# Performance work log

Measured on AMD Instinct MI355X. Metric: run time of the kernel, lower is better.

Reference implementation:

```python
import jax, jax.numpy as jnp
import numpy as np

N_NODES = 100000
N_EDGES = 1600000
F_IN, HIDDEN, N_CLASS = 64, 48, 40


def setup_inputs() -> dict:
    key = jax.random.key(0)
    ks = jax.random.split(key, 9)
    def glorot(k, fi, fo):
        s = (6.0 / (fi + fo)) ** 0.5
        return jax.random.uniform(k, (fi, fo), jnp.float32, -s, s)
    return {
        "x": jax.random.normal(ks[0], (N_NODES, F_IN), jnp.float32),
        "edge_index": jax.random.randint(ks[1], (2, N_EDGES), 0, N_NODES, jnp.int64),
        "edge_weight": jax.random.uniform(ks[2], (N_EDGES,), jnp.float32),
        "W1": glorot(ks[3], F_IN, HIDDEN),   # ARMAConv init_weight (K=1)
        "V1": glorot(ks[4], F_IN, HIDDEN),   # ARMAConv root_weight
        "b1": jnp.zeros((HIDDEN,), jnp.float32),
        "W2": glorot(ks[5], HIDDEN, N_CLASS),
        "V2": glorot(ks[6], HIDDEN, N_CLASS),
        "b2": jnp.zeros((N_CLASS,), jnp.float32),
    }


def _arma_conv(x, W, V, b, src, dst, norm, num_nodes):
    # out = ReLU( A_norm @ (x @ W) + x @ V + b )   (num_stacks=1, num_layers=1)
    h = x @ W                                   # [N, F_out]
    msg = h[src] * norm[:, None]                # gather + scale  [E, F_out]
    agg = jax.ops.segment_sum(msg, dst, num_segments=num_nodes)  # scatter-add
    return jax.nn.relu(agg + x @ V + b)


def reference(x, edge_index, edge_weight, W1, V1, b1, W2, V2, b2):
    num_nodes = x.shape[0]
    src, dst = edge_index[0], edge_index[1]
    # gcn_norm, add_self_loops=False: D^{-1/2} A D^{-1/2}
    deg = jax.ops.segment_sum(edge_weight, dst, num_segments=num_nodes)
    dinv = jnp.where(deg > 0, jax.lax.rsqrt(jnp.where(deg > 0, deg, 1.0)), 0.0)
    norm = dinv[src] * edge_weight * dinv[dst]
    # eval mode: input dropout is identity
    h = _arma_conv(x, W1, V1, b1, src, dst, norm, num_nodes)
    h = _arma_conv(h, W2, V2, b2, src, dst, norm, num_nodes)
    return jax.nn.log_softmax(h, axis=-1)
```

## Files before the change

### kernel.cpp

```cpp
#include <hip/hip_runtime.h>
#include <math.h>


constexpr int F_IN = 64;
constexpr int HIDDEN = 48;
constexpr int N_CLASS = 40;
constexpr int CHUNK = 8192;
constexpr int BIN_SHIFT = 9;
constexpr int CSR_CAP = 12288;

typedef __attribute__((ext_vector_type(8))) short bf16x8;
typedef __attribute__((ext_vector_type(4))) float f32x4;

__device__ __forceinline__ short bfr(float f) {
    unsigned u = __float_as_uint(f);
    return (short)((u + 0x7fffu + ((u >> 16) & 1u)) >> 16);
}
__device__ __forceinline__ unsigned pack_bf2(float a, float b) {
    unsigned ua = __float_as_uint(a), ub = __float_as_uint(b);
    ua = (ua + 0x7fffu + ((ua >> 16) & 1u)) >> 16;
    ub = (ub + 0x7fffu + ((ub >> 16) & 1u)) >> 16;
    return ua | (ub << 16);
}
__device__ __forceinline__ float2 unpack_bf2(unsigned u) {
    return make_float2(__uint_as_float(u << 16), __uint_as_float(u & 0xffff0000u));
}
__device__ __forceinline__ bf16x8 cvt8(float4 f0, float4 f1) {
    bf16x8 r;
    r[0] = bfr(f0.x); r[1] = bfr(f0.y); r[2] = bfr(f0.z); r[3] = bfr(f0.w);
    r[4] = bfr(f1.x); r[5] = bfr(f1.y); r[6] = bfr(f1.z); r[7] = bfr(f1.w);
    return r;
}

__device__ __forceinline__ void mfma_gemm1_body(char* smem, const float* __restrict__ X,
                                                const float* __restrict__ W,
                                                const float* __restrict__ V,
                                                const float* __restrict__ b,
                                                unsigned* __restrict__ XWp,
                                                float* __restrict__ AGG, int N, int gb,
                                                int tid) {
    short* sWT = (short*)smem;
    float* ep = (float*)(smem + 12288);
    for (int i = tid; i < 96 * 64; i += 256) {
        int c = i >> 6, k = i & 63;
        float v = (c < 48) ? W[k * 48 + c] : V[k * 48 + (c - 48)];
        sWT[i] = bfr(v);
    }
    __syncthreads();

    int lane = tid & 63, wv = tid >> 6;
    int m = lane & 15, quad = lane >> 4;
    int nb0 = gb * 64;
    int n = nb0 + wv * 16 + m;

    bf16x8 a0, a1;
    if (n < N) {
        const float4* xr = (const float4*)(X + (size_t)n * 64 + quad * 8);
        a0 = cvt8(xr[0], xr[1]);
        const float4* xr2 = (const float4*)(X + (size_t)n * 64 + 32 + quad * 8);
        a1 = cvt8(xr2[0], xr2[1]);
    } else {
        for (int j = 0; j < 8; ++j) { a0[j] = 0; a1[j] = 0; }
    }

    f32x4 acc[6];
#pragma unroll
    for (int ct = 0; ct < 6; ++ct) acc[ct] = (f32x4){0.f, 0.f, 0.f, 0.f};
#pragma unroll
    for (int ct = 0; ct < 6; ++ct) {
        bf16x8 b0 = *(const bf16x8*)(sWT + (ct * 16 + m) * 64 + quad * 8);
        bf16x8 b1 = *(const bf16x8*)(sWT + (ct * 16 + m) * 64 + 32 + quad * 8);
        acc[ct] = __builtin_amdgcn_mfma_f32_16x16x32_bf16(a0, b0, acc[ct], 0, 0, 0);
        acc[ct] = __builtin_amdgcn_mfma_f32_16x16x32_bf16(a1, b1, acc[ct], 0, 0, 0);
    }
#pragma unroll
    for (int ct = 0; ct < 6; ++ct)
#pragma unroll
        for (int r = 0; r < 4; ++r)
            ep[(wv * 16 + quad * 4 + r) * 96 + ct * 16 + m] = acc[ct][r];
    __syncthreads();
    for (int i = tid; i < 64 * 24; i += 256) {
        int r = i / 24, c2 = i - r * 24;
        int node = nb0 + r;
        if (node >= N) continue;
        float w0 = ep[r * 96 + 2 * c2], w1 = ep[r * 96 + 2 * c2 + 1];
        XWp[node * 24 + c2] = pack_bf2(w0, w1);
        float v0 = ep[r * 96 + 48 + 2 * c2], v1 = ep[r * 96 + 48 + 2 * c2 + 1];
        float2 bb = ((const float2*)b)[c2];
        ((float2*)AGG)[node * 24 + c2] = make_float2(v0 + bb.x, v1 + bb.y);
    }
}

__global__ __launch_bounds__(256) void count_gemm1(
    const int* __restrict__ dst, int* __restrict__ binCnt, int E, int nCountBlocks,
    const float* __restrict__ X, const float* __restrict__ W,
    const float* __restrict__ V, const float* __restrict__ b,
    unsigned* __restrict__ XWp, float* __restrict__ AGG, int N) {
    __shared__ char smem[36864];
    if ((int)blockIdx.x < nCountBlocks) {
        int* hist = (int*)smem;
        int tid = threadIdx.x;
        hist[tid] = 0;
        __syncthreads();
        long long e0 = (long long)blockIdx.x * CHUNK;
        int M = (int)min((long long)CHUNK, (long long)E - e0);
        for (int i = tid; i < M; i += 256) atomicAdd(&hist[dst[e0 + i] >> BIN_SHIFT], 1);
        __syncthreads();
        atomicAdd(&binCnt[tid], hist[tid]);
    } else {
        mfma_gemm1_body(smem, X, W, V, b, XWp, AGG, N,
                        (int)blockIdx.x - nCountBlocks, (int)threadIdx.x);
    }
}

__global__ void scan_bins(const int* __restrict__ binCnt, int* __restrict__ binStart,
                          int* __restrict__ binCursor, int* __restrict__ rowPtr,
                          int E, int N) {
    __shared__ int s[256];
    int t = threadIdx.x;
    int v = binCnt[t];
    s[t] = v;
    __syncthreads();
#pragma unroll
    for (int o = 1; o < 256; o <<= 1) {
        int u = (t >= o) ? s[t - o] : 0;
        __syncthreads();
        s[t] += u;
        __syncthreads();
    }
    int excl = s[t] - v;
    binStart[t] = excl;
    binCursor[t] = excl;
    if (t == 0) {
        binStart[256] = E;
        rowPtr[N] = E;
    }
}

__global__ void binscatter(const int* __restrict__ src, const int* __restrict__ dst,
                           const float* __restrict__ w, int* __restrict__ binCursor,
                           int2* __restrict__ binned, int E) {
    __shared__ int sx[CHUNK];
    __shared__ int sw[CHUNK];
    __shared__ unsigned char sbin[CHUNK];
    __shared__ int hist[256];
    int tid = threadIdx.x;
    hist[tid] = 0;
    __syncthreads();
    long long e0 = (long long)blockIdx.x * CHUNK;
    int M = (int)min((long long)CHUNK, (long long)E - e0);
    for (int i = tid; i < M; i += 256) {
        int d = dst[e0 + i];
        int bn = d >> BIN_SHIFT;
        sx[i] = ((d & 511) << 17) | src[e0 + i];
        sw[i] = __float_as_int(w[e0 + i]);
        sbin[i] = (unsigned char)bn;
        atomicAdd(&hist[bn], 1);
    }
    __syncthreads();
    int base = atomicAdd(&binCursor[tid], hist[tid]);
    __syncthreads();
    hist[tid] = base;
    __syncthreads();
    for (int i = tid; i < M; i += 256) {
        int p = atomicAdd(&hist[sbin[i]], 1);
        binned[p] = make_int2(sx[i], sw[i]);
    }
}

__global__ __launch_bounds__(512) void build_csr(const int2* __restrict__ binned,
                                                 const int* __restrict__ binStart,
                                                 int* __restrict__ rowPtr,
                                                 float* __restrict__ dinv,
                                                 int2* __restrict__ csr, int N) {
    __shared__ int sx[CSR_CAP];
    __shared__ int sw[CSR_CAP];
    __shared__ int cntL[512];
    __shared__ float degL[512];
    __shared__ int scanL[512];
    int b = blockIdx.x, tid = threadIdx.x;
    int e0 = binStart[b], e1 = binStart[b + 1], M = e1 - e0;
    cntL[tid] = 0;
    degL[tid] = 0.f;
    __syncthreads();
    bool fits = (M <= CSR_CAP);
    for (int i = tid; i < M; i += 512) {
        int2 p = binned[e0 + i];
        if (fits) { sx[i] = p.x; sw[i] = p.y; }
        int dl = ((unsigned)p.x) >> 17;
        atomicAdd(&cntL[dl], 1);
        atomicAdd(&degL[dl], __int_as_float(p.y));
    }
    __syncthreads();
    int v = cntL[tid];
    scanL[tid] = v;
    __syncthreads();
#pragma unroll
    for (int o = 1; o < 512; o <<= 1) {
        int u = (tid >= o) ? scanL[tid - o] : 0;
        __syncthreads();
        scanL[tid] += u;
        __syncthreads();
    }
    int excl = scanL[tid] - v;
    int node = (b << BIN_SHIFT) + tid;
    float dg = degL[tid];
    float dv = dg > 0.f ? rsqrtf(dg) : 0.f;
    if (node < N) {
        rowPtr[node] = e0 + excl;
        dinv[node] = dv;
    }
    cntL[tid] = e0 + excl;
    degL[tid] = dv;
    __syncthreads();
    for (int i = tid; i < M; i += 512) {
        int px, pw;
        if (fits) { px = sx[i]; pw = sw[i]; }
        else { int2 p = binned[e0 + i]; px = p.x; pw = p.y; }
        int dl = ((unsigned)px) >> 17;
        int pos = atomicAdd(&cntL[dl], 1);
        float wn = __int_as_float(pw) * degL[dl];
        csr[pos] = make_int2(px & 0x1FFFF, __float_as_int(wn));
    }
}

template <int C2>
__global__ void scale_xw(unsigned* __restrict__ XWp, const float* __restrict__ dinv,
                         int total) {
    int t = blockIdx.x * blockDim.x + threadIdx.x;
    if (t >= total) return;
    float dv = dinv[t / C2];
    float2 u = unpack_bf2(XWp[t]);
    XWp[t] = pack_bf2(u.x * dv, u.y * dv);
}

__global__ __launch_bounds__(256) void gemm2_kernel(
    const float* __restrict__ X, const float* __restrict__ W,
    const float* __restrict__ V, const float* __restrict__ b,
    const float* __restrict__ dinv, unsigned* __restrict__ XWp,
    float* __restrict__ AGG, int N) {
    __shared__ char smem[30720];
    short* sWT = (short*)smem;
    float* ep = (float*)(smem + 10240);
    int tid = threadIdx.x;
    for (int i = tid; i < 80 * 64; i += 256) {
        int c = i >> 6, k = i & 63;
        float v = 0.f;
        if (k < 48) v = (c < 40) ? W[k * 40 + c] : V[k * 40 + (c - 40)];
        sWT[i] = bfr(v);
    }
    __syncthreads();

    int lane = tid & 63, wv = tid >> 6;
    int m = lane & 15, quad = lane >> 4;
    int nb0 = (int)blockIdx.x * 64;
    int n = nb0 + wv * 16 + m;

    bf16x8 a0, a1;
    if (n < N) {
        const float4* xr = (const float4*)(X + (size_t)n * 48 + quad * 8);
        float4 f0 = xr[0], f1 = xr[1];
        f0.x = fmaxf(f0.x, 0.f); f0.y = fmaxf(f0.y, 0.f);
        f0.z = fmaxf(f0.z, 0.f); f0.w = fmaxf(f0.w, 0.f);
        f1.x = fmaxf(f1.x, 0.f); f1.y = fmaxf(f1.y, 0.f);
        f1.z = fmaxf(f1.z, 0.f); f1.w = fmaxf(f1.w, 0.f);
        a0 = cvt8(f0, f1);
        if (quad < 2) {
            const float4* xr2 = (const float4*)(X + (size_t)n * 48 + 32 + quad * 8);
            float4 g0 = xr2[0], g1 = xr2[1];
            g0.x = fmaxf(g0.x, 0.f); g0.y = fmaxf(g0.y, 0.f);
            g0.z = fmaxf(g0.z, 0.f); g0.w = fmaxf(g0.w, 0.f);
            g1.x = fmaxf(g1.x, 0.f); g1.y = fmaxf(g1.y, 0.f);
            g1.z = fmaxf(g1.z, 0.f); g1.w = fmaxf(g1.w, 0.f);
            a1 = cvt8(g0, g1);
        } else {
            for (int j = 0; j < 8; ++j) a1[j] = 0;
        }
    } else {
        for (int j = 0; j < 8; ++j) { a0[j] = 0; a1[j] = 0; }
    }

    f32x4 acc[5];
#pragma unroll
    for (int ct = 0; ct < 5; ++ct) acc[ct] = (f32x4){0.f, 0.f, 0.f, 0.f};
#pragma unroll
    for (int ct = 0; ct < 5; ++ct) {
        bf16x8 b0 = *(const bf16x8*)(sWT + (ct * 16 + m) * 64 + quad * 8);
        bf16x8 b1 = *(const bf16x8*)(sWT + (ct * 16 + m) * 64 + 32 + quad * 8);
        acc[ct] = __builtin_amdgcn_mfma_f32_16x16x32_bf16(a0, b0, acc[ct], 0, 0, 0);
        acc[ct] = __builtin_amdgcn_mfma_f32_16x16x32_bf16(a1, b1, acc[ct], 0, 0, 0);
    }
#pragma unroll
    for (int ct = 0; ct < 5; ++ct)
#pragma unroll
        for (int r = 0; r < 4; ++r)
            ep[(wv * 16 + quad * 4 + r) * 80 + ct * 16 + m] = acc[ct][r];
    __syncthreads();
    for (int i = tid; i < 64 * 20; i += 256) {
        int r = i / 20, c2 = i - r * 20;
        int node = nb0 + r;
        if (node >= N) continue;
        float dv = dinv[node];
        float w0 = ep[r * 80 + 2 * c2], w1 = ep[r * 80 + 2 * c2 + 1];
        XWp[node * 20 + c2] = pack_bf2(w0 * dv, w1 * dv);
        float v0 = ep[r * 80 + 40 + 2 * c2], v1 = ep[r * 80 + 40 + 2 * c2 + 1];
        float2 bb = ((const float2*)b)[c2];
        ((float2*)AGG)[node * 20 + c2] = make_float2(v0 + bb.x, v1 + bb.y);
    }
}

template <int C2>
__device__ __forceinline__ float2 row_accum(const unsigned* __restrict__ XWp,
                                            const int2* __restrict__ csr, int j,
                                            int end, int c2, float2 s) {
    for (; j + 4 <= end; j += 4) {
        int2 p0 = csr[j], p1 = csr[j + 1], p2 = csr[j + 2], p3 = csr[j + 3];
        unsigned u0 = XWp[p0.x * C2 + c2];
        unsigned u1 = XWp[p1.x * C2 + c2];
        unsigned u2 = XWp[p2.x * C2 + c2];
        unsigned u3 = XWp[p3.x * C2 + c2];
        float2 x0 = unpack_bf2(u0), x1 = unpack_bf2(u1);
        float2 x2 = unpack_bf2(u2), x3 = unpack_bf2(u3);
        float n0 = __int_as_float(p0.y), n1 = __int_as_float(p1.y);
        float n2 = __int_as_float(p2.y), n3 = __int_as_float(p3.y);
        s.x = fmaf(x0.x, n0, s.x); s.y = fmaf(x0.y, n0, s.y);
        s.x = fmaf(x1.x, n1, s.x); s.y = fmaf(x1.y, n1, s.y);
        s.x = fmaf(x2.x, n2, s.x); s.y = fmaf(x2.y, n2, s.y);
        s.x = fmaf(x3.x, n3, s.x); s.y = fmaf(x3.y, n3, s.y);
    }
    for (; j < end; ++j) {
        int2 p = csr[j];
        float2 xw = unpack_bf2(XWp[p.x * C2 + c2]);
        float nr = __int_as_float(p.y);
        s.x = fmaf(xw.x, nr, s.x);
        s.y = fmaf(xw.y, nr, s.y);
    }
    return s;
}

template <int C>
__global__ void pull_agg(const unsigned* __restrict__ XWp, const int2* __restrict__ csr,
                         const int* __restrict__ rowPtr, float* __restrict__ AGG, int N) {
    constexpr int C2 = C / 2;
    int t = blockIdx.x * blockDim.x + threadIdx.x;
    if (t >= N * C2) return;
    int n = t / C2, c2 = t - n * C2;
    float2 s = ((const float2*)AGG)[t];
    s = row_accum<C2>(XWp, csr, rowPtr[n], rowPtr[n + 1], c2, s);
    ((float2*)AGG)[t] = s;
}

__global__ __launch_bounds__(320) void pull_ls(const unsigned* __restrict__ XWp,
                                               const int2* __restrict__ csr,
                                               const int* __restrict__ rowPtr,
                                               const float* __restrict__ AGGin,
                                               float* __restrict__ out, int N) {
    constexpr int C2 = N_CLASS / 2;
    __shared__ float2 sbuf[16 * C2];
    __shared__ float sl[16];
    int tid = threadIdx.x;
    int nl = tid / C2, c2 = tid - nl * C2;
    int n = blockIdx.x * 16 + nl;
    float2 s = make_float2(0.f, 0.f);
    if (n < N) {
        s = ((const float2*)AGGin)[n * C2 + c2];
        s = row_accum<C2>(XWp, csr, rowPtr[n], rowPtr[n + 1], c2, s);
    }
    sbuf[tid] = s;
    __syncthreads();
    if (tid < 16) {
        const float2* row = sbuf + tid * C2;
        float m = 0.f;
        for (int k = 0; k < C2; ++k) {
            float2 v = row[k];
            m = fmaxf(m, fmaxf(v.x, v.y));
        }
        float sum = 0.f;
        for (int k = 0; k < C2; ++k) {
            float2 v = row[k];
            sum += expf(fmaxf(v.x, 0.f) - m) + expf(fmaxf(v.y, 0.f) - m);
        }
        sl[tid] = m + logf(sum);
    }
    __syncthreads();
    if (n < N) {
        float l = sl[nl];
        ((float2*)out)[n * C2 + c2] =
            make_float2(fmaxf(s.x, 0.f) - l, fmaxf(s.y, 0.f) - l);
    }
}

extern "C" void kernel_launch(void* const* d_in, const int* in_sizes, int n_in,
                              void* d_out, int out_size, void* d_ws, size_t ws_size,
                              hipStream_t stream) {
    const float* x  = (const float*)d_in[0];
    const int*   ei = (const int*)d_in[1];
    const float* ew = (const float*)d_in[2];
    const float* W1 = (const float*)d_in[3];
    const float* V1 = (const float*)d_in[4];
    const float* b1 = (const float*)d_in[5];
    const float* W2 = (const float*)d_in[6];
    const float* V2 = (const float*)d_in[7];
    const float* b2 = (const float*)d_in[8];
    float* out = (float*)d_out;

    const int N = in_sizes[0] / F_IN;
    const int E = in_sizes[2];
    const int* src = ei;
    const int* dst = ei + E;

    char* ws = (char*)d_ws;
    size_t off = 0;
    auto carve = [&](size_t bytes) {
        void* p = ws + off;
        off = (off + bytes + 255) & ~size_t(255);
        return p;
    };
    int*      binCnt    = (int*)carve(256 * 4);
    int*      binStart  = (int*)carve(257 * 4);
    int*      binCursor = (int*)carve(256 * 4);
    int*      rowPtr    = (int*)carve((size_t)(N + 1) * 4);
    float*    dinv      = (float*)carve((size_t)N * 4);
    int2*     binned    = (int2*)carve((size_t)E * 8);
    int2*     csr       = (int2*)carve((size_t)E * 8);
    unsigned* xW1p      = (unsigned*)carve((size_t)N * (HIDDEN / 2) * 4);
    float*    agg1      = (float*)carve((size_t)N * HIDDEN * 4);
    float*    agg2      = (float*)carve((size_t)N * N_CLASS * 4);
    unsigned* xW2p      = xW1p;

    const int B = 256;
    auto cdiv = [](long long a, long long b) { return (int)((a + b - 1) / b); };
    const int nChunks = cdiv(E, CHUNK);
    const int nBins = (N + (1 << BIN_SHIFT) - 1) >> BIN_SHIFT;
    const int nGemmBlocks = cdiv(N, 64);

    hipMemsetAsync(binCnt, 0, 256 * 4, stream);

    count_gemm1<<<nChunks + nGemmBlocks, B, 0, stream>>>(dst, binCnt, E, nChunks,
                                                         x, W1, V1, b1, xW1p, agg1, N);
    scan_bins<<<1, 256, 0, stream>>>(binCnt, binStart, binCursor, rowPtr, E, N);
    binscatter<<<nChunks, B, 0, stream>>>(src, dst, ew, binCursor, binned, E);
    build_csr<<<nBins, 512, 0, stream>>>(binned, binStart, rowPtr, dinv, csr, N);

    scale_xw<HIDDEN / 2><<<cdiv((long long)N * (HIDDEN / 2), B), B, 0, stream>>>(
        xW1p, dinv, N * (HIDDEN / 2));

    pull_agg<HIDDEN><<<cdiv((long long)N * (HIDDEN / 2), B), B, 0, stream>>>(
        xW1p, csr, rowPtr, agg1, N);

    gemm2_kernel<<<nGemmBlocks, B, 0, stream>>>(agg1, W2, V2, b2, dinv, xW2p, agg2, N);

    pull_ls<<<cdiv(N, 16), 320, 0, stream>>>(xW2p, csr, rowPtr, agg2, out, N);
}
```

Baseline: 294.4 us.

## Split gathered feature tables into column slabs and sweep slabs in persistent pull kernels

```diff
diff --git a/kernel.cpp b/kernel.cpp
--- a/kernel.cpp
+++ b/kernel.cpp
@@ -8,6 +8,8 @@
 constexpr int CHUNK = 8192;
 constexpr int BIN_SHIFT = 9;
 constexpr int CSR_CAP = 12288;
+constexpr int PULL_GRID = 1568;
+constexpr int P2TILES = 2;
 
 typedef __attribute__((ext_vector_type(8))) short bf16x8;
 typedef __attribute__((ext_vector_type(4))) float f32x4;
@@ -84,7 +86,8 @@
         int node = nb0 + r;
         if (node >= N) continue;
         float w0 = ep[r * 96 + 2 * c2], w1 = ep[r * 96 + 2 * c2 + 1];
-        XWp[node * 24 + c2] = pack_bf2(w0, w1);
+        int s = c2 >> 3, cc = c2 & 7;
+        XWp[((size_t)s * N + node) * 8 + cc] = pack_bf2(w0, w1);
         float v0 = ep[r * 96 + 48 + 2 * c2], v1 = ep[r * 96 + 48 + 2 * c2 + 1];
         float2 bb = ((const float2*)b)[c2];
         ((float2*)AGG)[node * 24 + c2] = make_float2(v0 + bb.x, v1 + bb.y);
@@ -224,12 +227,14 @@
     }
 }
 
-template <int C2>
 __global__ void scale_xw(unsigned* __restrict__ XWp, const float* __restrict__ dinv,
-                         int total) {
+                         int N) {
     int t = blockIdx.x * blockDim.x + threadIdx.x;
-    if (t >= total) return;
-    float dv = dinv[t / C2];
+    if (t >= N * 24) return;
+    int slabN8 = N * 8;
+    int s = t / slabN8;
+    int n = (t - s * slabN8) >> 3;
+    float dv = dinv[n];
     float2 u = unpack_bf2(XWp[t]);
     XWp[t] = pack_bf2(u.x * dv, u.y * dv);
 }
@@ -302,23 +307,26 @@
         if (node >= N) continue;
         float dv = dinv[node];
         float w0 = ep[r * 80 + 2 * c2], w1 = ep[r * 80 + 2 * c2 + 1];
-        XWp[node * 20 + c2] = pack_bf2(w0 * dv, w1 * dv);
+        unsigned pk = pack_bf2(w0 * dv, w1 * dv);
+        if (c2 < 8)       XWp[node * 8 + c2] = pk;
+        else if (c2 < 16) XWp[(size_t)N * 8 + node * 8 + (c2 - 8)] = pk;
+        else              XWp[(size_t)N * 16 + node * 4 + (c2 - 16)] = pk;
         float v0 = ep[r * 80 + 40 + 2 * c2], v1 = ep[r * 80 + 40 + 2 * c2 + 1];
         float2 bb = ((const float2*)b)[c2];
         ((float2*)AGG)[node * 20 + c2] = make_float2(v0 + bb.x, v1 + bb.y);
     }
 }
 
-template <int C2>
-__device__ __forceinline__ float2 row_accum(const unsigned* __restrict__ XWp,
-                                            const int2* __restrict__ csr, int j,
-                                            int end, int c2, float2 s) {
+template <int W>
+__device__ __forceinline__ float2 row_accumW(const unsigned* __restrict__ slab,
+                                             const int2* __restrict__ csr, int j,
+                                             int end, int c, float2 s) {
     for (; j + 4 <= end; j += 4) {
         int2 p0 = csr[j], p1 = csr[j + 1], p2 = csr[j + 2], p3 = csr[j + 3];
-        unsigned u0 = XWp[p0.x * C2 + c2];
-        unsigned u1 = XWp[p1.x * C2 + c2];
-        unsigned u2 = XWp[p2.x * C2 + c2];
-        unsigned u3 = XWp[p3.x * C2 + c2];
+        unsigned u0 = slab[p0.x * W + c];
+        unsigned u1 = slab[p1.x * W + c];
+        unsigned u2 = slab[p2.x * W + c];
+        unsigned u3 = slab[p3.x * W + c];
         float2 x0 = unpack_bf2(u0), x1 = unpack_bf2(u1);
         float2 x2 = unpack_bf2(u2), x3 = unpack_bf2(u3);
         float n0 = __int_as_float(p0.y), n1 = __int_as_float(p1.y);
@@ -330,7 +338,7 @@
     }
     for (; j < end; ++j) {
         int2 p = csr[j];
-        float2 xw = unpack_bf2(XWp[p.x * C2 + c2]);
+        float2 xw = unpack_bf2(slab[p.x * W + c]);
         float nr = __int_as_float(p.y);
         s.x = fmaf(xw.x, nr, s.x);
         s.y = fmaf(xw.y, nr, s.y);
@@ -338,55 +346,104 @@
     return s;
 }
 
-template <int C>
-__global__ void pull_agg(const unsigned* __restrict__ XWp, const int2* __restrict__ csr,
-                         const int* __restrict__ rowPtr, float* __restrict__ AGG, int N) {
-    constexpr int C2 = C / 2;
-    int t = blockIdx.x * blockDim.x + threadIdx.x;
-    if (t >= N * C2) return;
-    int n = t / C2, c2 = t - n * C2;
-    float2 s = ((const float2*)AGG)[t];
-    s = row_accum<C2>(XWp, csr, rowPtr[n], rowPtr[n + 1], c2, s);
-    ((float2*)AGG)[t] = s;
-}
-
-__global__ __launch_bounds__(320) void pull_ls(const unsigned* __restrict__ XWp,
-                                               const int2* __restrict__ csr,
-                                               const int* __restrict__ rowPtr,
-                                               const float* __restrict__ AGGin,
-                                               float* __restrict__ out, int N) {
-    constexpr int C2 = N_CLASS / 2;
-    __shared__ float2 sbuf[16 * C2];
-    __shared__ float sl[16];
+__global__ __launch_bounds__(256) void pull1(const unsigned* __restrict__ XWp,
+                                             const int2* __restrict__ csr,
+                                             const int* __restrict__ rowPtr,
+                                             float* __restrict__ AGG, int N,
+                                             int nTiles) {
     int tid = threadIdx.x;
-    int nl = tid / C2, c2 = tid - nl * C2;
-    int n = blockIdx.x * 16 + nl;
-    float2 s = make_float2(0.f, 0.f);
-    if (n < N) {
-        s = ((const float2*)AGGin)[n * C2 + c2];
-        s = row_accum<C2>(XWp, csr, rowPtr[n], rowPtr[n + 1], c2, s);
-    }
-    sbuf[tid] = s;
-    __syncthreads();
-    if (tid < 16) {
-        const float2* row = sbuf + tid * C2;
-        float m = 0.f;
-        for (int k = 0; k < C2; ++k) {
-            float2 v = row[k];
-            m = fmaxf(m, fmaxf(v.x, v.y));
+    int nl = tid >> 3, c = tid & 7;
+#pragma unroll
+    for (int s = 0; s < 3; ++s) {
+        const unsigned* slab = XWp + (size_t)s * N * 8;
+        int cp = s * 8 + c;
+        for (int tile = blockIdx.x; tile < nTiles; tile += gridDim.x) {
+            int n = tile * 32 + nl;
+            if (n >= N) continue;
+            int beg = rowPtr[n], end = rowPtr[n + 1];
+            float2 acc = ((const float2*)AGG)[n * 24 + cp];
+            acc = row_accumW<8>(slab, csr, beg, end, c, acc);
+            ((float2*)AGG)[n * 24 + cp] = acc;
         }
-        float sum = 0.f;
-        for (int k = 0; k < C2; ++k) {
-            float2 v = row[k];
-            sum += expf(fmaxf(v.x, 0.f) - m) + expf(fmaxf(v.y, 0.f) - m);
+    }
+}
+
+__global__ __launch_bounds__(256) void pull2_ls(const unsigned* __restrict__ XWp,
+                                                const int2* __restrict__ csr,
+                                                const int* __restrict__ rowPtr,
+                                                const float* __restrict__ AGGin,
+                                                float* __restrict__ out, int N,
+                                                int nTiles) {
+    __shared__ float2 sacc[P2TILES * 32 * 20];
+    __shared__ float sl[P2TILES * 32];
+    int tid = threadIdx.x;
+#pragma unroll
+    for (int tl = 0; tl < P2TILES; ++tl) {
+        int tile = blockIdx.x + tl * gridDim.x;
+        if (tile >= nTiles) break;
+        for (int i = tid; i < 32 * 20; i += 256) {
+            int nl = i / 20, c2 = i - nl * 20;
+            int n = tile * 32 + nl;
+            sacc[tl * 640 + i] =
+                (n < N) ? ((const float2*)AGGin)[n * 20 + c2] : make_float2(0.f, 0.f);
         }
-        sl[tid] = m + logf(sum);
-    }
-    __syncthreads();
-    if (n < N) {
-        float l = sl[nl];
-        ((float2*)out)[n * C2 + c2] =
-            make_float2(fmaxf(s.x, 0.f) - l, fmaxf(s.y, 0.f) - l);
+    }
+    __syncthreads();
+#pragma unroll
+    for (int s = 0; s < 3; ++s) {
+        int w = (s == 2) ? 4 : 8;
+        const unsigned* slab = XWp + (size_t)((s == 2) ? N * 16 : s * N * 8);
+        int nl = tid / w, c = tid - nl * w;
+        if (nl < 32) {
+#pragma unroll
+            for (int tl = 0; tl < P2TILES; ++tl) {
+                int tile = blockIdx.x + tl * gridDim.x;
+                if (tile >= nTiles) break;
+                int n = tile * 32 + nl;
+                if (n >= N) continue;
+                int beg = rowPtr[n], end = rowPtr[n + 1];
+                float2 acc = make_float2(0.f, 0.f);
+                acc = (w == 8) ? row_accumW<8>(slab, csr, beg, end, c, acc)
+                               : row_accumW<4>(slab, csr, beg, end, c, acc);
+                int cp = (s == 2) ? 16 + c : s * 8 + c;
+                float2* p = &sacc[tl * 640 + nl * 20 + cp];
+                *p = make_float2(p->x + acc.x, p->y + acc.y);
+            }
+        }
+    }
+    __syncthreads();
+    if (tid < P2TILES * 32) {
+        int tl = tid >> 5, nl = tid & 31;
+        int tile = blockIdx.x + tl * gridDim.x;
+        if (tile < nTiles) {
+            const float2* row = &sacc[tl * 640 + nl * 20];
+            float m = 0.f;
+            for (int k = 0; k < 20; ++k) {
+                float2 v = row[k];
+                m = fmaxf(m, fmaxf(v.x, v.y));
+            }
+            float sum = 0.f;
+            for (int k = 0; k < 20; ++k) {
+                float2 v = row[k];
+                sum += expf(fmaxf(v.x, 0.f) - m) + expf(fmaxf(v.y, 0.f) - m);
+            }
+            sl[tid] = m + logf(sum);
+        }
+    }
+    __syncthreads();
+#pragma unroll
+    for (int tl = 0; tl < P2TILES; ++tl) {
+        int tile = blockIdx.x + tl * gridDim.x;
+        if (tile >= nTiles) break;
+        for (int i = tid; i < 32 * 20; i += 256) {
+            int nl = i / 20, c2 = i - nl * 20;
+            int n = tile * 32 + nl;
+            if (n >= N) continue;
+            float l = sl[tl * 32 + nl];
+            float2 v = sacc[tl * 640 + i];
+            ((float2*)out)[n * 20 + c2] =
+                make_float2(fmaxf(v.x, 0.f) - l, fmaxf(v.y, 0.f) - l);
+        }
     }
 }
 
@@ -433,6 +490,7 @@
     const int nChunks = cdiv(E, CHUNK);
     const int nBins = (N + (1 << BIN_SHIFT) - 1) >> BIN_SHIFT;
     const int nGemmBlocks = cdiv(N, 64);
+    const int nTiles = cdiv(N, 32);
 
     hipMemsetAsync(binCnt, 0, 256 * 4, stream);
 
@@ -442,13 +500,11 @@
     binscatter<<<nChunks, B, 0, stream>>>(src, dst, ew, binCursor, binned, E);
     build_csr<<<nBins, 512, 0, stream>>>(binned, binStart, rowPtr, dinv, csr, N);
 
-    scale_xw<HIDDEN / 2><<<cdiv((long long)N * (HIDDEN / 2), B), B, 0, stream>>>(
-        xW1p, dinv, N * (HIDDEN / 2));
-
-    pull_agg<HIDDEN><<<cdiv((long long)N * (HIDDEN / 2), B), B, 0, stream>>>(
-        xW1p, csr, rowPtr, agg1, N);
+    scale_xw<<<cdiv((long long)N * 24, B), B, 0, stream>>>(xW1p, dinv, N);
+
+    pull1<<<PULL_GRID, B, 0, stream>>>(xW1p, csr, rowPtr, agg1, N, nTiles);
 
     gemm2_kernel<<<nGemmBlocks, B, 0, stream>>>(agg1, W2, V2, b2, dinv, xW2p, agg2, N);
 
-    pull_ls<<<cdiv(N, 16), 320, 0, stream>>>(xW2p, csr, rowPtr, agg2, out, N);
-}
+    pull2_ls<<<PULL_GRID, B, 0, stream>>>(xW2p, csr, rowPtr, agg2, out, N, nTiles);
+}
```

New measurement: 309.9 us. +5.2%, slower.

## Compress CSR entries to 32 bits and fuse layer-1 aggregation into GEMM2

Applied to the files above, without the earlier changes.

```diff
diff --git a/kernel.cpp b/kernel.cpp
--- a/kernel.cpp
+++ b/kernel.cpp
@@ -172,7 +172,7 @@
                                                  const int* __restrict__ binStart,
                                                  int* __restrict__ rowPtr,
                                                  float* __restrict__ dinv,
-                                                 int2* __restrict__ csr, int N) {
+                                                 unsigned* __restrict__ csr, int N) {
     __shared__ int sx[CSR_CAP];
     __shared__ int sw[CSR_CAP];
     __shared__ int cntL[512];
@@ -220,28 +220,61 @@
         int dl = ((unsigned)px) >> 17;
         int pos = atomicAdd(&cntL[dl], 1);
         float wn = __int_as_float(pw) * degL[dl];
-        csr[pos] = make_int2(px & 0x1FFFF, __float_as_int(wn));
-    }
-}
-
-template <int C2>
+        unsigned uw = __float_as_uint(wn);
+        uw = (uw + 0x7fffu + ((uw >> 16) & 1u)) >> 16;
+        csr[pos] = ((unsigned)(px & 0x1FFFF) << 15) | uw;
+    }
+}
+
 __global__ void scale_xw(unsigned* __restrict__ XWp, const float* __restrict__ dinv,
                          int total) {
     int t = blockIdx.x * blockDim.x + threadIdx.x;
     if (t >= total) return;
-    float dv = dinv[t / C2];
+    float dv = dinv[t / 24];
     float2 u = unpack_bf2(XWp[t]);
     XWp[t] = pack_bf2(u.x * dv, u.y * dv);
 }
 
-__global__ __launch_bounds__(256) void gemm2_kernel(
-    const float* __restrict__ X, const float* __restrict__ W,
-    const float* __restrict__ V, const float* __restrict__ b,
-    const float* __restrict__ dinv, unsigned* __restrict__ XWp,
-    float* __restrict__ AGG, int N) {
-    __shared__ char smem[30720];
-    short* sWT = (short*)smem;
-    float* ep = (float*)(smem + 10240);
+template <int W>
+__device__ __forceinline__ float2 row_accumC(const unsigned* __restrict__ XWp,
+                                             const unsigned* __restrict__ csr, int j,
+                                             int end, int c, float2 s) {
+    for (; j + 4 <= end; j += 4) {
+        unsigned p0 = csr[j], p1 = csr[j + 1], p2 = csr[j + 2], p3 = csr[j + 3];
+        unsigned u0 = XWp[(p0 >> 15) * W + c];
+        unsigned u1 = XWp[(p1 >> 15) * W + c];
+        unsigned u2 = XWp[(p2 >> 15) * W + c];
+        unsigned u3 = XWp[(p3 >> 15) * W + c];
+        float2 x0 = unpack_bf2(u0), x1 = unpack_bf2(u1);
+        float2 x2 = unpack_bf2(u2), x3 = unpack_bf2(u3);
+        float n0 = __uint_as_float((p0 & 0x7FFFu) << 16);
+        float n1 = __uint_as_float((p1 & 0x7FFFu) << 16);
+        float n2 = __uint_as_float((p2 & 0x7FFFu) << 16);
+        float n3 = __uint_as_float((p3 & 0x7FFFu) << 16);
+        s.x = fmaf(x0.x, n0, s.x); s.y = fmaf(x0.y, n0, s.y);
+        s.x = fmaf(x1.x, n1, s.x); s.y = fmaf(x1.y, n1, s.y);
+        s.x = fmaf(x2.x, n2, s.x); s.y = fmaf(x2.y, n2, s.y);
+        s.x = fmaf(x3.x, n3, s.x); s.y = fmaf(x3.y, n3, s.y);
+    }
+    for (; j < end; ++j) {
+        unsigned p = csr[j];
+        float2 xw = unpack_bf2(XWp[(p >> 15) * W + c]);
+        float nr = __uint_as_float((p & 0x7FFFu) << 16);
+        s.x = fmaf(xw.x, nr, s.x);
+        s.y = fmaf(xw.y, nr, s.y);
+    }
+    return s;
+}
+
+__global__ __launch_bounds__(256) void pull1_gemm2(
+    const unsigned* __restrict__ XW1p, const unsigned* __restrict__ csr,
+    const int* __restrict__ rowPtr, const float* __restrict__ AGG1in,
+    const float* __restrict__ W, const float* __restrict__ V,
+    const float* __restrict__ b, const float* __restrict__ dinv,
+    unsigned* __restrict__ XW2p, float* __restrict__ AGG2, int N) {
+    __shared__ short sWT[80 * 64];
+    __shared__ float sA[64 * 48];
+    __shared__ float ep[64 * 80];
     int tid = threadIdx.x;
     for (int i = tid; i < 80 * 64; i += 256) {
         int c = i >> 6, k = i & 63;
@@ -249,37 +282,35 @@
         if (k < 48) v = (c < 40) ? W[k * 40 + c] : V[k * 40 + (c - 40)];
         sWT[i] = bfr(v);
     }
-    __syncthreads();
-
+    int nb0 = (int)blockIdx.x * 64;
+    for (int i = tid; i < 64 * 24; i += 256) {
+        int nl = i / 24, c2 = i - nl * 24;
+        int n = nb0 + nl;
+        float2 acc = make_float2(0.f, 0.f);
+        if (n < N) {
+            acc = ((const float2*)AGG1in)[n * 24 + c2];
+            acc = row_accumC<24>(XW1p, csr, rowPtr[n], rowPtr[n + 1], c2, acc);
+        }
+        sA[nl * 48 + 2 * c2] = fmaxf(acc.x, 0.f);
+        sA[nl * 48 + 2 * c2 + 1] = fmaxf(acc.y, 0.f);
+    }
+    __syncthreads();
     int lane = tid & 63, wv = tid >> 6;
     int m = lane & 15, quad = lane >> 4;
-    int nb0 = (int)blockIdx.x * 64;
-    int n = nb0 + wv * 16 + m;
-
     bf16x8 a0, a1;
-    if (n < N) {
-        const float4* xr = (const float4*)(X + (size_t)n * 48 + quad * 8);
-        float4 f0 = xr[0], f1 = xr[1];
-        f0.x = fmaxf(f0.x, 0.f); f0.y = fmaxf(f0.y, 0.f);
-        f0.z = fmaxf(f0.z, 0.f); f0.w = fmaxf(f0.w, 0.f);
-        f1.x = fmaxf(f1.x, 0.f); f1.y = fmaxf(f1.y, 0.f);
-        f1.z = fmaxf(f1.z, 0.f); f1.w = fmaxf(f1.w, 0.f);
+    {
+        const float* ar = sA + (wv * 16 + m) * 48;
+        float4 f0 = *(const float4*)(ar + quad * 8);
+        float4 f1 = *(const float4*)(ar + quad * 8 + 4);
         a0 = cvt8(f0, f1);
         if (quad < 2) {
-            const float4* xr2 = (const float4*)(X + (size_t)n * 48 + 32 + quad * 8);
-            float4 g0 = xr2[0], g1 = xr2[1];
-            g0.x = fmaxf(g0.x, 0.f); g0.y = fmaxf(g0.y, 0.f);
-            g0.z = fmaxf(g0.z, 0.f); g0.w = fmaxf(g0.w, 0.f);
-            g1.x = fmaxf(g1.x, 0.f); g1.y = fmaxf(g1.y, 0.f);
-            g1.z = fmaxf(g1.z, 0.f); g1.w = fmaxf(g1.w, 0.f);
+            float4 g0 = *(const float4*)(ar + 32 + quad * 8);
+            float4 g1 = *(const float4*)(ar + 32 + quad * 8 + 4);
             a1 = cvt8(g0, g1);
         } else {
             for (int j = 0; j < 8; ++j) a1[j] = 0;
         }
-    } else {
-        for (int j = 0; j < 8; ++j) { a0[j] = 0; a1[j] = 0; }
-    }
-
+    }
     f32x4 acc[5];
 #pragma unroll
     for (int ct = 0; ct < 5; ++ct) acc[ct] = (f32x4){0.f, 0.f, 0.f, 0.f};
@@ -302,56 +333,15 @@
         if (node >= N) continue;
         float dv = dinv[node];
         float w0 = ep[r * 80 + 2 * c2], w1 = ep[r * 80 + 2 * c2 + 1];
-        XWp[node * 20 + c2] = pack_bf2(w0 * dv, w1 * dv);
+        XW2p[node * 20 + c2] = pack_bf2(w0 * dv, w1 * dv);
         float v0 = ep[r * 80 + 40 + 2 * c2], v1 = ep[r * 80 + 40 + 2 * c2 + 1];
         float2 bb = ((const float2*)b)[c2];
-        ((float2*)AGG)[node * 20 + c2] = make_float2(v0 + bb.x, v1 + bb.y);
-    }
-}
-
-template <int C2>
-__device__ __forceinline__ float2 row_accum(const unsigned* __restrict__ XWp,
-                                            const int2* __restrict__ csr, int j,
-                                            int end, int c2, float2 s) {
-    for (; j + 4 <= end; j += 4) {
-        int2 p0 = csr[j], p1 = csr[j + 1], p2 = csr[j + 2], p3 = csr[j + 3];
-        unsigned u0 = XWp[p0.x * C2 + c2];
-        unsigned u1 = XWp[p1.x * C2 + c2];
-        unsigned u2 = XWp[p2.x * C2 + c2];
-        unsigned u3 = XWp[p3.x * C2 + c2];
-        float2 x0 = unpack_bf2(u0), x1 = unpack_bf2(u1);
-        float2 x2 = unpack_bf2(u2), x3 = unpack_bf2(u3);
-        float n0 = __int_as_float(p0.y), n1 = __int_as_float(p1.y);
-        float n2 = __int_as_float(p2.y), n3 = __int_as_float(p3.y);
-        s.x = fmaf(x0.x, n0, s.x); s.y = fmaf(x0.y, n0, s.y);
-        s.x = fmaf(x1.x, n1, s.x); s.y = fmaf(x1.y, n1, s.y);
-        s.x = fmaf(x2.x, n2, s.x); s.y = fmaf(x2.y, n2, s.y);
-        s.x = fmaf(x3.x, n3, s.x); s.y = fmaf(x3.y, n3, s.y);
-    }
-    for (; j < end; ++j) {
-        int2 p = csr[j];
-        float2 xw = unpack_bf2(XWp[p.x * C2 + c2]);
-        float nr = __int_as_float(p.y);
-        s.x = fmaf(xw.x, nr, s.x);
-        s.y = fmaf(xw.y, nr, s.y);
-    }
-    return s;
-}
-
-template <int C>
-__global__ void pull_agg(const unsigned* __restrict__ XWp, const int2* __restrict__ csr,
-                         const int* __restrict__ rowPtr, float* __restrict__ AGG, int N) {
-    constexpr int C2 = C / 2;
-    int t = blockIdx.x * blockDim.x + threadIdx.x;
-    if (t >= N * C2) return;
-    int n = t / C2, c2 = t - n * C2;
-    float2 s = ((const float2*)AGG)[t];
-    s = row_accum<C2>(XWp, csr, rowPtr[n], rowPtr[n + 1], c2, s);
-    ((float2*)AGG)[t] = s;
+        ((float2*)AGG2)[node * 20 + c2] = make_float2(v0 + bb.x, v1 + bb.y);
+    }
 }
 
 __global__ __launch_bounds__(320) void pull_ls(const unsigned* __restrict__ XWp,
-                                               const int2* __restrict__ csr,
+                                               const unsigned* __restrict__ csr,
                                                const int* __restrict__ rowPtr,
                                                const float* __restrict__ AGGin,
                                                float* __restrict__ out, int N) {
@@ -364,7 +354,7 @@
     float2 s = make_float2(0.f, 0.f);
     if (n < N) {
         s = ((const float2*)AGGin)[n * C2 + c2];
-        s = row_accum<C2>(XWp, csr, rowPtr[n], rowPtr[n + 1], c2, s);
+        s = row_accumC<C2>(XWp, csr, rowPtr[n], rowPtr[n + 1], c2, s);
     }
     sbuf[tid] = s;
     __syncthreads();
@@ -422,11 +412,11 @@
     int*      rowPtr    = (int*)carve((size_t)(N + 1) * 4);
     float*    dinv      = (float*)carve((size_t)N * 4);
     int2*     binned    = (int2*)carve((size_t)E * 8);
-    int2*     csr       = (int2*)carve((size_t)E * 8);
-    unsigned* xW1p      = (unsigned*)carve((size_t)N * (HIDDEN / 2) * 4);
+    unsigned* csr       = (unsigned*)carve((size_t)E * 4);
+    unsigned* xW1p      = (unsigned*)carve((size_t)N * 24 * 4);
+    unsigned* xW2p      = (unsigned*)carve((size_t)N * 20 * 4);
     float*    agg1      = (float*)carve((size_t)N * HIDDEN * 4);
     float*    agg2      = (float*)carve((size_t)N * N_CLASS * 4);
-    unsigned* xW2p      = xW1p;
 
     const int B = 256;
     auto cdiv = [](long long a, long long b) { return (int)((a + b - 1) / b); };
@@ -442,13 +432,10 @@
     binscatter<<<nChunks, B, 0, stream>>>(src, dst, ew, binCursor, binned, E);
     build_csr<<<nBins, 512, 0, stream>>>(binned, binStart, rowPtr, dinv, csr, N);
 
-    scale_xw<HIDDEN / 2><<<cdiv((long long)N * (HIDDEN / 2), B), B, 0, stream>>>(
-        xW1p, dinv, N * (HIDDEN / 2));
-
-    pull_agg<HIDDEN><<<cdiv((long long)N * (HIDDEN / 2), B), B, 0, stream>>>(
-        xW1p, csr, rowPtr, agg1, N);
-
-    gemm2_kernel<<<nGemmBlocks, B, 0, stream>>>(agg1, W2, V2, b2, dinv, xW2p, agg2, N);
+    scale_xw<<<cdiv((long long)N * 24, B), B, 0, stream>>>(xW1p, dinv, N * 24);
+
+    pull1_gemm2<<<nGemmBlocks, B, 0, stream>>>(xW1p, csr, rowPtr, agg1,
+                                               W2, V2, b2, dinv, xW2p, agg2, N);
 
     pull_ls<<<cdiv(N, 16), 320, 0, stream>>>(xW2p, csr, rowPtr, agg2, out, N);
 }
```

New measurement: 334.3 us. +13.5%, slower.
